# Optimization experiments

Hardware: AMD Instinct MI355X
Metric: run time of the kernel (lower is better)

Reference implementation:

```python
import jax, jax.numpy as jnp
import numpy as np

B, T, C, H = 4, 2048, 1024, 16
HD = C // H  # head_dim = 64


def setup_inputs() -> dict:
    key = jax.random.key(0)
    k1, k2, k3 = jax.random.split(key, 3)
    x = jax.random.normal(k1, (B, T, C), dtype=jnp.float32)
    W_qkv = jax.random.normal(k2, (C, 3 * C), dtype=jnp.float32) * (1.0 / np.sqrt(C))
    W_out = jax.random.normal(k3, (C, C), dtype=jnp.float32) * (1.0 / np.sqrt(C))
    return {"x": x, "W_qkv": W_qkv, "W_out": W_out}


def reference(x, W_qkv, W_out):
    Bx, Tx, Cx = x.shape
    qkv = jnp.einsum('btc,cd->btd', x, W_qkv)  # [B,T,3C]
    q, k, v = jnp.split(qkv, 3, axis=-1)
    # [B,T,C] -> [B,H,T,HD]
    q = q.reshape(Bx, Tx, H, HD).transpose(0, 2, 1, 3)
    k = k.reshape(Bx, Tx, H, HD).transpose(0, 2, 1, 3)
    v = v.reshape(Bx, Tx, H, HD).transpose(0, 2, 1, 3)
    scale = 1.0 / jnp.sqrt(jnp.asarray(HD, dtype=x.dtype))
    attn = jnp.einsum('bhqd,bhkd->bhqk', q, k) * scale  # [B,H,T,T]
    causal = jnp.tril(jnp.ones((Tx, Tx), dtype=bool))
    attn = jnp.where(causal, attn, jnp.asarray(-1e9, dtype=attn.dtype))
    attn = jax.nn.softmax(attn, axis=-1)
    out = jnp.einsum('bhqk,bhkd->bhqd', attn, v)  # [B,H,T,HD]
    out = out.transpose(0, 2, 1, 3).reshape(Bx, Tx, Cx)
    return jnp.einsum('btc,cd->btd', out, W_out)
```

## Files before the change

### kernel.cpp

```cpp
#include <hip/hip_runtime.h>
#include <hip/hip_bf16.h>
#include <cstdint>


typedef __attribute__((ext_vector_type(8))) short bf16x8;
typedef __attribute__((ext_vector_type(4))) float f32x4;
typedef __attribute__((ext_vector_type(4))) uint32_t u32x4;

#define MFMA_BF16(a, b, c) __builtin_amdgcn_mfma_f32_16x16x32_bf16((a), (b), (c), 0, 0, 0)

__device__ __forceinline__ ushort f2bf(float f) {
  union { float f; uint32_t u; } x;
  x.f = f;
  uint32_t u = x.u;
  return (ushort)((u + 0x7FFFu + ((u >> 16) & 1u)) >> 16);
}

__device__ __forceinline__ uint32_t cvt_pk_bf16(float lo, float hi) {
  uint32_t r;
  asm("v_cvt_pk_bf16_f32 %0, %1, %2" : "=v"(r) : "v"(lo), "v"(hi));
  return r;
}

__device__ __forceinline__ void gload16(const ushort* g, ushort* l) {
  __builtin_amdgcn_global_load_lds(
      (const __attribute__((address_space(1))) void*)g,
      (__attribute__((address_space(3))) void*)l, 16, 0, 0);
}

__global__ __launch_bounds__(256) void convert_f32_bf16(
    const float* __restrict__ in, ushort* __restrict__ out, int n4) {
  int i = blockIdx.x * 256 + threadIdx.x;
  if (i < n4) {
    float4 v = ((const float4*)in)[i];
    ushort4 o;
    o.x = f2bf(v.x); o.y = f2bf(v.y); o.z = f2bf(v.z); o.w = f2bf(v.w);
    ((ushort4*)out)[i] = o;
  }
}

__global__ __launch_bounds__(256) void transpose_w(
    const float* __restrict__ W, ushort* __restrict__ Wt, int K, int N) {
  __shared__ float tile[32][33];
  const int n0 = blockIdx.x * 32, k0 = blockIdx.y * 32;
  const int tx = threadIdx.x & 31, ty = threadIdx.x >> 5;
#pragma unroll
  for (int i = 0; i < 4; ++i)
    tile[ty + i * 8][tx] = W[(size_t)(k0 + ty + i * 8) * N + n0 + tx];
  __syncthreads();
#pragma unroll
  for (int i = 0; i < 4; ++i)
    Wt[(size_t)(n0 + ty + i * 8) * K + k0 + tx] = f2bf(tile[tx][ty + i * 8]);
}

template <int MODE>
__global__ __launch_bounds__(256)
__attribute__((amdgpu_waves_per_eu(2, 2)))
void gemm_bf16_kernel(
    const ushort* __restrict__ A, const ushort* __restrict__ Bt,
    float* __restrict__ C,
    ushort* __restrict__ qb, ushort* __restrict__ kb, ushort* __restrict__ vb,
    int M, int N, int K) {
  __shared__ ushort As[2][128 * 64];
  __shared__ ushort Bs[2][128 * 64];
  const int tid = threadIdx.x;
  const int lane = tid & 63;
  const int w = tid >> 6;
  const int wr = w >> 1, wc = w & 1;
  const int l15 = lane & 15, lhi = lane >> 4;
  const int row0 = blockIdx.x * 128, col0 = blockIdx.y * 128;

  const int cr = lane >> 3;
  const int sl = lane & 7;
  const int gofs = (sl ^ cr) << 3;
  const ushort* gA = A  + (size_t)(row0 + w * 32 + cr) * K + gofs;
  const ushort* gB = Bt + (size_t)(col0 + w * 32 + cr) * K + gofs;
  const int lbase = (w * 32) * 64;

  f32x4 acc[4][4] = {};

#define G_STAGE(BUF, K0)                                                     \
  {                                                                          \
    _Pragma("unroll")                                                        \
    for (int i = 0; i < 4; ++i) {                                            \
      gload16(gA + (size_t)(i * 8) * K + (K0), &As[BUF][lbase + i * 512]);   \
      gload16(gB + (size_t)(i * 8) * K + (K0), &Bs[BUF][lbase + i * 512]);   \
    }                                                                        \
  }

  const int nk = K >> 6;
  G_STAGE(0, 0)
  __syncthreads();

  for (int t = 0; t < nk; ++t) {
    const int cur = t & 1;
    if (t + 1 < nk) G_STAGE(cur ^ 1, (t + 1) << 6)

#pragma unroll
    for (int kh = 0; kh < 2; ++kh) {
      bf16x8 af[4], bfr[4];
#pragma unroll
      for (int m = 0; m < 4; ++m) {
        const int row = wr * 64 + m * 16 + l15;
        const int s = kh * 4 + lhi;
        af[m] = *(const bf16x8*)&As[cur][row * 64 + ((s ^ (row & 7)) << 3)];
      }
#pragma unroll
      for (int n = 0; n < 4; ++n) {
        const int row = wc * 64 + n * 16 + l15;
        const int s = kh * 4 + lhi;
        bfr[n] = *(const bf16x8*)&Bs[cur][row * 64 + ((s ^ (row & 7)) << 3)];
      }
      __builtin_amdgcn_s_setprio(1);
#pragma unroll
      for (int m = 0; m < 4; ++m)
#pragma unroll
        for (int n = 0; n < 4; ++n)
          acc[m][n] = MFMA_BF16(af[m], bfr[n], acc[m][n]);
      __builtin_amdgcn_s_setprio(0);
    }
    __syncthreads();
  }
#undef G_STAGE

  if (MODE == 1) {
#pragma unroll
    for (int m = 0; m < 4; ++m) {
      const int r0 = row0 + wr * 64 + m * 16 + lhi * 4;
#pragma unroll
      for (int n = 0; n < 4; ++n) {
        const int c = col0 + wc * 64 + n * 16 + l15;
#pragma unroll
        for (int j = 0; j < 4; ++j)
          C[(size_t)(r0 + j) * N + c] = acc[m][n][j];
      }
    }
  } else {
    const float QSCALE = 0.18033688011112042f;
#pragma unroll
    for (int m = 0; m < 4; ++m) {
      const int r0 = row0 + wr * 64 + m * 16 + lhi * 4;
      const int b_ = r0 >> 11;
      const int t0 = r0 & 2047;
#pragma unroll
      for (int n = 0; n < 4; ++n) {
        const int c = col0 + wc * 64 + n * 16 + l15;
        const int seg = c >> 10;
        const int cc = c & 1023;
        const int h = cc >> 6, d = cc & 63;
        const size_t bhi = (size_t)(b_ * 16 + h);
        if (seg == 0) {
#pragma unroll
          for (int j = 0; j < 4; ++j)
            qb[(bhi * 2048 + t0 + j) * 64 + d] = f2bf(acc[m][n][j] * QSCALE);
        } else if (seg == 1) {
#pragma unroll
          for (int j = 0; j < 4; ++j)
            kb[(bhi * 2048 + t0 + j) * 64 + d] = f2bf(acc[m][n][j]);
        } else {
          const int pos = (t0 & ~31) + ((t0 & 12) << 1) + ((t0 >> 4) & 1) * 4;
          ushort4 pk;
          pk.x = f2bf(acc[m][n][0]);
          pk.y = f2bf(acc[m][n][1]);
          pk.z = f2bf(acc[m][n][2]);
          pk.w = f2bf(acc[m][n][3]);
          *(ushort4*)(vb + (bhi * 64 + d) * 2048 + pos) = pk;
        }
      }
    }
  }
}

#define QK_TILE(SV, KT)                                                      \
  {                                                                          \
    const int krow = (KT) * 16 + l15;                                        \
    const int sw = krow & 7;                                                 \
    bf16x8 kf0 = *(const bf16x8*)&Ks[cur][krow * 64 + ((lhi ^ sw) * 8)];     \
    bf16x8 kf1 = *(const bf16x8*)&Ks[cur][krow * 64 + (((4 + lhi) ^ sw) * 8)];\
    f32x4 acc_ = {};                                                         \
    acc_ = MFMA_BF16(kf0, qf0, acc_);                                        \
    acc_ = MFMA_BF16(kf1, qf1, acc_);                                        \
    SV = acc_;                                                               \
  }

#define MASK_TILE(SV, KT)                                                    \
  {                                                                          \
    if (key0 + (KT) * 16 + lhi * 4 + 0 > qrow) SV[0] = -INFINITY;            \
    if (key0 + (KT) * 16 + lhi * 4 + 1 > qrow) SV[1] = -INFINITY;            \
    if (key0 + (KT) * 16 + lhi * 4 + 2 > qrow) SV[2] = -INFINITY;            \
    if (key0 + (KT) * 16 + lhi * 4 + 3 > qrow) SV[3] = -INFINITY;            \
  }

#define SM_TILE(SV, W0, W1)                                                  \
  {                                                                          \
    float p0 = exp2f(SV[0] - m_state);                                       \
    float p1 = exp2f(SV[1] - m_state);                                       \
    float p2 = exp2f(SV[2] - m_state);                                       \
    float p3 = exp2f(SV[3] - m_state);                                       \
    lloc += (p0 + p1) + (p2 + p3);                                           \
    W0 = cvt_pk_bf16(p0, p1);                                                \
    W1 = cvt_pk_bf16(p2, p3);                                                \
  }

#define PV_TILE(ON, N)                                                       \
  {                                                                          \
    const int vrow = (N) * 16 + l15;                                         \
    const int sw = vrow & 7;                                                 \
    bf16x8 vf0 = *(const bf16x8*)&Vs[cur][vrow * 64 + ((lhi ^ sw) * 8)];     \
    bf16x8 vf1 = *(const bf16x8*)&Vs[cur][vrow * 64 + (((4 + lhi) ^ sw) * 8)];\
    ON = MFMA_BF16(pf0, vf0, ON);                                            \
    ON = MFMA_BF16(pf1, vf1, ON);                                            \
  }

__global__ __launch_bounds__(256)
__attribute__((amdgpu_waves_per_eu(4, 4)))
void attn_kernel(
    const ushort* __restrict__ Qb, const ushort* __restrict__ Kb,
    const ushort* __restrict__ Vt, ushort* __restrict__ Ab) {
  const int bid = blockIdx.x;
  const int qt = 31 - (bid >> 6);
  const int bh = bid & 63;
  const int tid = threadIdx.x;
  const int lane = tid & 63;
  const int w = tid >> 6;
  const int l15 = lane & 15, lhi = lane >> 4;
  const int qloc = qt * 64 + w * 16;

  __shared__ ushort Ks[2][64 * 64];
  __shared__ ushort Vs[2][64 * 64];

  const size_t qkbase = (size_t)bh * (2048 * 64);
  const size_t vtb = (size_t)bh * (64 * 2048);

  const int srow = w * 16 + (lane >> 3);
  const int sd0 = lane & 7;
  const int slot = (sd0 ^ (srow & 7)) * 8;

  const ushort* kp0 = Kb + qkbase + (size_t)srow * 64 + sd0 * 8;
  const ushort* kp1 = kp0 + 8 * 64;
  const ushort* vp0 = Vt + vtb + (size_t)srow * 2048 + sd0 * 8;
  const ushort* vp1 = vp0 + 8 * 2048;

  bf16x8 qf0 = *(const bf16x8*)(Qb + qkbase + (size_t)(qloc + l15) * 64 + lhi * 8);
  bf16x8 qf1 = *(const bf16x8*)(Qb + qkbase + (size_t)(qloc + l15) * 64 + 32 + lhi * 8);

  uint4 kr0 = *(const uint4*)kp0;
  uint4 kr1 = *(const uint4*)kp1;
  uint4 vr0 = *(const uint4*)vp0;
  uint4 vr1 = *(const uint4*)vp1;
  *(uint4*)&Ks[0][srow * 64 + slot] = kr0;
  *(uint4*)&Ks[0][(srow + 8) * 64 + slot] = kr1;
  *(uint4*)&Vs[0][srow * 64 + slot] = vr0;
  *(uint4*)&Vs[0][(srow + 8) * 64 + slot] = vr1;
  __syncthreads();

  float m_state = -INFINITY, l_state = 0.f;
  f32x4 o0 = {}, o1 = {}, o2 = {}, o3 = {};
  const int qrow = qloc + l15;
  int cur = 0;

  for (int kbt = 0; kbt <= qt; ++kbt) {
    const int key0 = kbt * 64;
    const bool last = (kbt == qt);

    if (!last) {
      const size_t koff = (size_t)(kbt + 1) * 64 * 64;
      kr0 = *(const uint4*)(kp0 + koff);
      kr1 = *(const uint4*)(kp1 + koff);
      vr0 = *(const uint4*)(vp0 + (kbt + 1) * 64);
      vr1 = *(const uint4*)(vp1 + (kbt + 1) * 64);
    }

    f32x4 s0, s1, s2, s3;
    __builtin_amdgcn_s_setprio(1);
    QK_TILE(s0, 0)
    QK_TILE(s1, 1)
    QK_TILE(s2, 2)
    QK_TILE(s3, 3)
    __builtin_amdgcn_s_setprio(0);

    if (last) {
      MASK_TILE(s0, 0)
      MASK_TILE(s1, 1)
      MASK_TILE(s2, 2)
      MASK_TILE(s3, 3)
    }

    float t0 = fmaxf(fmaxf(s0[0], s0[1]), fmaxf(s0[2], s0[3]));
    float t1 = fmaxf(fmaxf(s1[0], s1[1]), fmaxf(s1[2], s1[3]));
    float t2 = fmaxf(fmaxf(s2[0], s2[1]), fmaxf(s2[2], s2[3]));
    float t3 = fmaxf(fmaxf(s3[0], s3[1]), fmaxf(s3[2], s3[3]));
    float tmax = fmaxf(fmaxf(t0, t1), fmaxf(t2, t3));
    tmax = fmaxf(tmax, __shfl_xor(tmax, 16));
    tmax = fmaxf(tmax, __shfl_xor(tmax, 32));

    if (!__all(tmax <= m_state + 8.0f)) {
      const float mnew = fmaxf(m_state, tmax);
      const float alpha = exp2f(m_state - mnew);
      const float a0 = __shfl(alpha, lhi * 4 + 0);
      const float a1 = __shfl(alpha, lhi * 4 + 1);
      const float a2 = __shfl(alpha, lhi * 4 + 2);
      const float a3 = __shfl(alpha, lhi * 4 + 3);
      o0[0] *= a0; o0[1] *= a1; o0[2] *= a2; o0[3] *= a3;
      o1[0] *= a0; o1[1] *= a1; o1[2] *= a2; o1[3] *= a3;
      o2[0] *= a0; o2[1] *= a1; o2[2] *= a2; o2[3] *= a3;
      o3[0] *= a0; o3[1] *= a1; o3[2] *= a2; o3[3] *= a3;
      l_state *= alpha;
      m_state = mnew;
    }

    float lloc = 0.f;
    uint32_t w0, w1, w2, w3, w4, w5, w6, w7;
    SM_TILE(s0, w0, w1)
    SM_TILE(s1, w2, w3)
    SM_TILE(s2, w4, w5)
    SM_TILE(s3, w6, w7)
    lloc += __shfl_xor(lloc, 16);
    lloc += __shfl_xor(lloc, 32);
    l_state += lloc;

    u32x4 pw0 = {w0, w1, w2, w3};
    u32x4 pw1 = {w4, w5, w6, w7};
    bf16x8 pf0 = __builtin_bit_cast(bf16x8, pw0);
    bf16x8 pf1 = __builtin_bit_cast(bf16x8, pw1);

    __builtin_amdgcn_s_setprio(1);
    PV_TILE(o0, 0)
    PV_TILE(o1, 1)
    PV_TILE(o2, 2)
    PV_TILE(o3, 3)
    __builtin_amdgcn_s_setprio(0);

    if (!last) {
      const int nxt = cur ^ 1;
      *(uint4*)&Ks[nxt][srow * 64 + slot] = kr0;
      *(uint4*)&Ks[nxt][(srow + 8) * 64 + slot] = kr1;
      *(uint4*)&Vs[nxt][srow * 64 + slot] = vr0;
      *(uint4*)&Vs[nxt][(srow + 8) * 64 + slot] = vr1;
      cur = nxt;
      __syncthreads();
    }
  }

  const int b_ = bh >> 4, h_ = bh & 15;
#pragma unroll
  for (int j = 0; j < 4; ++j) {
    const float linv = 1.0f / __shfl(l_state, lhi * 4 + j);
    const int t = qloc + lhi * 4 + j;
    const size_t ro = ((size_t)b_ * 2048 + t) * 1024 + h_ * 64;
    Ab[ro + 0 * 16 + l15] = f2bf(o0[j] * linv);
    Ab[ro + 1 * 16 + l15] = f2bf(o1[j] * linv);
    Ab[ro + 2 * 16 + l15] = f2bf(o2[j] * linv);
    Ab[ro + 3 * 16 + l15] = f2bf(o3[j] * linv);
  }
}

extern "C" void kernel_launch(void* const* d_in, const int* in_sizes, int n_in,
                              void* d_out, int out_size, void* d_ws, size_t ws_size,
                              hipStream_t stream) {
  const float* x = (const float*)d_in[0];
  const float* Wqkv = (const float*)d_in[1];
  const float* Wout = (const float*)d_in[2];
  float* out = (float*)d_out;

  ushort* xb    = (ushort*)d_ws;
  ushort* wqkvT = xb + (size_t)8192 * 1024;
  ushort* woutT = wqkvT + (size_t)3072 * 1024;
  ushort* qb    = woutT + (size_t)1024 * 1024;
  ushort* kbuf  = qb + (size_t)64 * 2048 * 64;
  ushort* vbuf  = kbuf + (size_t)64 * 2048 * 64;
  ushort* ab    = vbuf + (size_t)64 * 2048 * 64;

  convert_f32_bf16<<<8192, 256, 0, stream>>>(x, xb, 8192 * 1024 / 4);
  transpose_w<<<dim3(96, 32), 256, 0, stream>>>(Wqkv, wqkvT, 1024, 3072);
  transpose_w<<<dim3(32, 32), 256, 0, stream>>>(Wout, woutT, 1024, 1024);
  gemm_bf16_kernel<0><<<dim3(64, 24), 256, 0, stream>>>(
      xb, wqkvT, nullptr, qb, kbuf, vbuf, 8192, 3072, 1024);
  attn_kernel<<<2048, 256, 0, stream>>>(qb, kbuf, vbuf, ab);
  gemm_bf16_kernel<1><<<dim3(64, 8), 256, 0, stream>>>(
      ab, woutT, out, nullptr, nullptr, nullptr, 8192, 1024, 1024);
}
```

Baseline: 173.8 us.

## Halve GEMM K-tile, raise occupancy to three waves, add XCD-aware block swizzle

```diff
diff --git a/kernel.cpp b/kernel.cpp
--- a/kernel.cpp
+++ b/kernel.cpp
@@ -55,71 +55,71 @@
 
 template <int MODE>
 __global__ __launch_bounds__(256)
-__attribute__((amdgpu_waves_per_eu(2, 2)))
+__attribute__((amdgpu_waves_per_eu(3, 3)))
 void gemm_bf16_kernel(
     const ushort* __restrict__ A, const ushort* __restrict__ Bt,
     float* __restrict__ C,
     ushort* __restrict__ qb, ushort* __restrict__ kb, ushort* __restrict__ vb,
     int M, int N, int K) {
-  __shared__ ushort As[2][128 * 64];
-  __shared__ ushort Bs[2][128 * 64];
+  __shared__ ushort As[2][128 * 32];
+  __shared__ ushort Bs[2][128 * 32];
   const int tid = threadIdx.x;
   const int lane = tid & 63;
   const int w = tid >> 6;
   const int wr = w >> 1, wc = w & 1;
   const int l15 = lane & 15, lhi = lane >> 4;
-  const int row0 = blockIdx.x * 128, col0 = blockIdx.y * 128;
-
-  const int cr = lane >> 3;
-  const int sl = lane & 7;
-  const int gofs = (sl ^ cr) << 3;
+
+  const int nwg = gridDim.x;
+  const int cpx = nwg >> 3;
+  const int b = blockIdx.x;
+  const int swz = (b & 7) * cpx + (b >> 3);
+  const int row0 = (swz & 63) * 128;
+  const int col0 = (swz >> 6) * 128;
+
+  const int cr = lane >> 2;
+  const int sl = lane & 3;
+  const int gofs = (sl ^ (cr & 3)) << 3;
   const ushort* gA = A  + (size_t)(row0 + w * 32 + cr) * K + gofs;
   const ushort* gB = Bt + (size_t)(col0 + w * 32 + cr) * K + gofs;
-  const int lbase = (w * 32) * 64;
+  const int lbase = (w * 32) * 32;
 
   f32x4 acc[4][4] = {};
 
-#define G_STAGE(BUF, K0)                                                     \
-  {                                                                          \
-    _Pragma("unroll")                                                        \
-    for (int i = 0; i < 4; ++i) {                                            \
-      gload16(gA + (size_t)(i * 8) * K + (K0), &As[BUF][lbase + i * 512]);   \
-      gload16(gB + (size_t)(i * 8) * K + (K0), &Bs[BUF][lbase + i * 512]);   \
-    }                                                                        \
-  }
-
-  const int nk = K >> 6;
+#define G_STAGE(BUF, T)                                                      \
+  {                                                                          \
+    gload16(gA + (size_t)(T) * 32, &As[BUF][lbase]);                         \
+    gload16(gA + (size_t)16 * K + (size_t)(T) * 32, &As[BUF][lbase + 512]);  \
+    gload16(gB + (size_t)(T) * 32, &Bs[BUF][lbase]);                         \
+    gload16(gB + (size_t)16 * K + (size_t)(T) * 32, &Bs[BUF][lbase + 512]);  \
+  }
+
+  const int nk = K >> 5;
   G_STAGE(0, 0)
   __syncthreads();
 
   for (int t = 0; t < nk; ++t) {
     const int cur = t & 1;
-    if (t + 1 < nk) G_STAGE(cur ^ 1, (t + 1) << 6)
-
-#pragma unroll
-    for (int kh = 0; kh < 2; ++kh) {
-      bf16x8 af[4], bfr[4];
-#pragma unroll
-      for (int m = 0; m < 4; ++m) {
-        const int row = wr * 64 + m * 16 + l15;
-        const int s = kh * 4 + lhi;
-        af[m] = *(const bf16x8*)&As[cur][row * 64 + ((s ^ (row & 7)) << 3)];
-      }
-#pragma unroll
-      for (int n = 0; n < 4; ++n) {
-        const int row = wc * 64 + n * 16 + l15;
-        const int s = kh * 4 + lhi;
-        bfr[n] = *(const bf16x8*)&Bs[cur][row * 64 + ((s ^ (row & 7)) << 3)];
-      }
-      __builtin_amdgcn_s_setprio(1);
-#pragma unroll
-      for (int m = 0; m < 4; ++m)
-#pragma unroll
-        for (int n = 0; n < 4; ++n)
-          acc[m][n] = MFMA_BF16(af[m], bfr[n], acc[m][n]);
-      __builtin_amdgcn_s_setprio(0);
-    }
-    __syncthreads();
+    if (t + 1 < nk) G_STAGE(cur ^ 1, t + 1)
+
+    bf16x8 af[4], bfr[4];
+#pragma unroll
+    for (int m = 0; m < 4; ++m) {
+      const int row = wr * 64 + m * 16 + l15;
+      af[m] = *(const bf16x8*)&As[cur][row * 32 + ((lhi ^ (row & 3)) << 3)];
+    }
+#pragma unroll
+    for (int n = 0; n < 4; ++n) {
+      const int row = wc * 64 + n * 16 + l15;
+      bfr[n] = *(const bf16x8*)&Bs[cur][row * 32 + ((lhi ^ (row & 3)) << 3)];
+    }
+    __builtin_amdgcn_s_setprio(1);
+#pragma unroll
+    for (int m = 0; m < 4; ++m)
+#pragma unroll
+      for (int n = 0; n < 4; ++n)
+        acc[m][n] = MFMA_BF16(af[m], bfr[n], acc[m][n]);
+    __builtin_amdgcn_s_setprio(0);
+    if (t + 1 < nk) __syncthreads();
   }
 #undef G_STAGE
 
@@ -374,9 +374,9 @@
   convert_f32_bf16<<<8192, 256, 0, stream>>>(x, xb, 8192 * 1024 / 4);
   transpose_w<<<dim3(96, 32), 256, 0, stream>>>(Wqkv, wqkvT, 1024, 3072);
   transpose_w<<<dim3(32, 32), 256, 0, stream>>>(Wout, woutT, 1024, 1024);
-  gemm_bf16_kernel<0><<<dim3(64, 24), 256, 0, stream>>>(
+  gemm_bf16_kernel<0><<<1536, 256, 0, stream>>>(
       xb, wqkvT, nullptr, qb, kbuf, vbuf, 8192, 3072, 1024);
   attn_kernel<<<2048, 256, 0, stream>>>(qb, kbuf, vbuf, ab);
-  gemm_bf16_kernel<1><<<dim3(64, 8), 256, 0, stream>>>(
+  gemm_bf16_kernel<1><<<512, 256, 0, stream>>>(
       ab, woutT, out, nullptr, nullptr, nullptr, 8192, 1024, 1024);
 }
```

New measurement: 193.4 us. 1.11x slower.

## Use 256x256-tile 8-wave QKV GEMM with staged loads and XCD-aware block mapping

Applied to the files above, without the earlier changes.

```diff
diff --git a/kernel.cpp b/kernel.cpp
--- a/kernel.cpp
+++ b/kernel.cpp
@@ -53,14 +53,190 @@
     Wt[(size_t)(n0 + ty + i * 8) * K + k0 + tx] = f2bf(tile[tx][ty + i * 8]);
 }
 
-template <int MODE>
+
+#define LD_AF(MH)                                                            \
+  {                                                                          \
+    _Pragma("unroll")                                                        \
+    for (int m = 0; m < 4; ++m) {                                            \
+      const int row = wr * 128 + (MH) * 64 + m * 16 + l15;                   \
+      _Pragma("unroll")                                                      \
+      for (int kk = 0; kk < 2; ++kk)                                         \
+        af[m][kk] = *(const bf16x8*)&as[row * 64 +                           \
+                     (((kk * 4 + lhi) ^ (row & 7)) << 3)];                   \
+    }                                                                        \
+  }
+
+#define LD_BF(DST, NH)                                                       \
+  {                                                                          \
+    _Pragma("unroll")                                                        \
+    for (int n = 0; n < 2; ++n) {                                            \
+      const int row = wc * 64 + (NH) * 32 + n * 16 + l15;                    \
+      _Pragma("unroll")                                                      \
+      for (int kk = 0; kk < 2; ++kk)                                         \
+        DST[n][kk] = *(const bf16x8*)&bs[row * 64 +                          \
+                     (((kk * 4 + lhi) ^ (row & 7)) << 3)];                   \
+    }                                                                        \
+  }
+
+#define MFMA16(MH, NH, BF)                                                   \
+  {                                                                          \
+    __builtin_amdgcn_s_setprio(1);                                           \
+    _Pragma("unroll")                                                        \
+    for (int m = 0; m < 4; ++m)                                              \
+      _Pragma("unroll")                                                      \
+      for (int n = 0; n < 2; ++n)                                            \
+        _Pragma("unroll")                                                    \
+        for (int kk = 0; kk < 2; ++kk)                                       \
+          acc[(MH) * 4 + m][(NH) * 2 + n] = MFMA_BF16(                       \
+              af[m][kk], BF[n][kk], acc[(MH) * 4 + m][(NH) * 2 + n]);        \
+    __builtin_amdgcn_s_setprio(0);                                           \
+  }
+
+__global__ __launch_bounds__(512)
+__attribute__((amdgpu_waves_per_eu(2, 2)))
+void gemm256_qkv(
+    const ushort* __restrict__ A, const ushort* __restrict__ Bt,
+    ushort* __restrict__ qb, ushort* __restrict__ kb, ushort* __restrict__ vb,
+    int M, int N, int K) {
+  __shared__ ushort As[2][256 * 64];
+  __shared__ ushort Bs[2][256 * 64];
+  const int tid = threadIdx.x;
+  const int lane = tid & 63;
+  const int w = tid >> 6;
+  const int wr = w >> 2, wc = w & 3;
+  const int l15 = lane & 15, lhi = lane >> 4;
+
+  const int ncolt = N >> 8;
+  const int rpx = (M >> 8) >> 3;
+  const int b = blockIdx.x;
+  const int xcd = b & 7;
+  const int loc = b >> 3;
+  const int rowg = loc / ncolt;
+  const int colt = loc - rowg * ncolt;
+  const int row0 = (xcd * rpx + rowg) * 256;
+  const int col0 = colt * 256;
+
+  const int cr8 = lane >> 3;
+  const int sl8 = lane & 7;
+  const int gcol = (sl8 ^ cr8) << 3;
+  const int rA = (w & 3) * 16 + (w >> 2) * 128;
+  const int rB = (w & 1) * 16 + (w >> 1) * 64;
+  const ushort* gA0u = A  + (size_t)(row0 + rA + cr8) * K + gcol;
+  const ushort* gB0u = Bt + (size_t)(col0 + rB + cr8) * K + gcol;
+  const ushort* gA1u = gA0u + (size_t)64 * K;
+  const ushort* gB1u = gB0u + (size_t)32 * K;
+  const int lA0 = rA * 64;
+  const int lB0 = rB * 64;
+  const int lA1 = lA0 + 64 * 64;
+  const int lB1 = lB0 + 32 * 64;
+
+#define STAGE_A0(BUF, T)                                                     \
+  { gload16(gA0u + (size_t)(T) * 64, &As[BUF][lA0]);                         \
+    gload16(gA0u + (size_t)8 * K + (size_t)(T) * 64, &As[BUF][lA0 + 512]); }
+#define STAGE_B0(BUF, T)                                                     \
+  { gload16(gB0u + (size_t)(T) * 64, &Bs[BUF][lB0]);                         \
+    gload16(gB0u + (size_t)8 * K + (size_t)(T) * 64, &Bs[BUF][lB0 + 512]); }
+#define STAGE_B1(BUF, T)                                                     \
+  { gload16(gB1u + (size_t)(T) * 64, &Bs[BUF][lB1]);                         \
+    gload16(gB1u + (size_t)8 * K + (size_t)(T) * 64, &Bs[BUF][lB1 + 512]); }
+#define STAGE_A1(BUF, T)                                                     \
+  { gload16(gA1u + (size_t)(T) * 64, &As[BUF][lA1]);                         \
+    gload16(gA1u + (size_t)8 * K + (size_t)(T) * 64, &As[BUF][lA1 + 512]); }
+
+  f32x4 acc[8][4] = {};
+
+  const int nk = K >> 6;
+  STAGE_A0(0, 0)
+  STAGE_B0(0, 0)
+  STAGE_B1(0, 0)
+  STAGE_A1(0, 0)
+
+  for (int t = 0; t < nk; ++t) {
+    const int cur = t & 1;
+    const int nxt = cur ^ 1;
+    const ushort* as = &As[cur][0];
+    const ushort* bs = &Bs[cur][0];
+    const bool pre = (t + 1 < nk);
+
+    bf16x8 af[4][2], bf0[2][2], bf1[2][2];
+
+    asm volatile("s_waitcnt vmcnt(4)" ::: "memory");
+    __builtin_amdgcn_s_barrier();
+    __builtin_amdgcn_sched_barrier(0);
+    LD_AF(0)
+    LD_BF(bf0, 0)
+    if (pre) STAGE_A0(nxt, t + 1)
+    MFMA16(0, 0, bf0)
+
+    if (pre) {
+      asm volatile("s_waitcnt vmcnt(4)" ::: "memory");
+    } else {
+      asm volatile("s_waitcnt vmcnt(2)" ::: "memory");
+    }
+    __builtin_amdgcn_s_barrier();
+    __builtin_amdgcn_sched_barrier(0);
+    LD_BF(bf1, 1)
+    if (pre) STAGE_B0(nxt, t + 1)
+    MFMA16(0, 1, bf1)
+
+    if (pre) {
+      asm volatile("s_waitcnt vmcnt(4)" ::: "memory");
+    } else {
+      asm volatile("s_waitcnt vmcnt(0)" ::: "memory");
+    }
+    __builtin_amdgcn_s_barrier();
+    __builtin_amdgcn_sched_barrier(0);
+    LD_AF(1)
+    if (pre) STAGE_B1(nxt, t + 1)
+    MFMA16(1, 1, bf1)
+
+    if (pre) STAGE_A1(nxt, t + 1)
+    MFMA16(1, 0, bf0)
+  }
+#undef STAGE_A0
+#undef STAGE_B0
+#undef STAGE_B1
+#undef STAGE_A1
+
+  const float QSCALE = 0.18033688011112042f;
+#pragma unroll
+  for (int m = 0; m < 8; ++m) {
+    const int r0 = row0 + wr * 128 + m * 16 + lhi * 4;
+    const int b_ = r0 >> 11;
+    const int t0 = r0 & 2047;
+#pragma unroll
+    for (int n = 0; n < 4; ++n) {
+      const int c = col0 + wc * 64 + n * 16 + l15;
+      const int seg = c >> 10;
+      const int cc = c & 1023;
+      const int h = cc >> 6, d = cc & 63;
+      const size_t bhi = (size_t)(b_ * 16 + h);
+      if (seg == 0) {
+#pragma unroll
+        for (int j = 0; j < 4; ++j)
+          qb[(bhi * 2048 + t0 + j) * 64 + d] = f2bf(acc[m][n][j] * QSCALE);
+      } else if (seg == 1) {
+#pragma unroll
+        for (int j = 0; j < 4; ++j)
+          kb[(bhi * 2048 + t0 + j) * 64 + d] = f2bf(acc[m][n][j]);
+      } else {
+        const int pos = (t0 & ~31) + ((t0 & 12) << 1) + ((t0 >> 4) & 1) * 4;
+        ushort4 pk;
+        pk.x = f2bf(acc[m][n][0]);
+        pk.y = f2bf(acc[m][n][1]);
+        pk.z = f2bf(acc[m][n][2]);
+        pk.w = f2bf(acc[m][n][3]);
+        *(ushort4*)(vb + (bhi * 64 + d) * 2048 + pos) = pk;
+      }
+    }
+  }
+}
+
 __global__ __launch_bounds__(256)
 __attribute__((amdgpu_waves_per_eu(2, 2)))
-void gemm_bf16_kernel(
+void gemm_out(
     const ushort* __restrict__ A, const ushort* __restrict__ Bt,
-    float* __restrict__ C,
-    ushort* __restrict__ qb, ushort* __restrict__ kb, ushort* __restrict__ vb,
-    int M, int N, int K) {
+    float* __restrict__ C, int M, int N, int K) {
   __shared__ ushort As[2][128 * 64];
   __shared__ ushort Bs[2][128 * 64];
   const int tid = threadIdx.x;
@@ -79,7 +255,7 @@
 
   f32x4 acc[4][4] = {};
 
-#define G_STAGE(BUF, K0)                                                     \
+#define G_STAGE8(BUF, K0)                                                    \
   {                                                                          \
     _Pragma("unroll")                                                        \
     for (int i = 0; i < 4; ++i) {                                            \
@@ -89,12 +265,12 @@
   }
 
   const int nk = K >> 6;
-  G_STAGE(0, 0)
+  G_STAGE8(0, 0)
   __syncthreads();
 
   for (int t = 0; t < nk; ++t) {
     const int cur = t & 1;
-    if (t + 1 < nk) G_STAGE(cur ^ 1, (t + 1) << 6)
+    if (t + 1 < nk) G_STAGE8(cur ^ 1, (t + 1) << 6)
 
 #pragma unroll
     for (int kh = 0; kh < 2; ++kh) {
@@ -121,52 +297,17 @@
     }
     __syncthreads();
   }
-#undef G_STAGE
-
-  if (MODE == 1) {
-#pragma unroll
-    for (int m = 0; m < 4; ++m) {
-      const int r0 = row0 + wr * 64 + m * 16 + lhi * 4;
-#pragma unroll
-      for (int n = 0; n < 4; ++n) {
-        const int c = col0 + wc * 64 + n * 16 + l15;
-#pragma unroll
-        for (int j = 0; j < 4; ++j)
-          C[(size_t)(r0 + j) * N + c] = acc[m][n][j];
-      }
-    }
-  } else {
-    const float QSCALE = 0.18033688011112042f;
-#pragma unroll
-    for (int m = 0; m < 4; ++m) {
-      const int r0 = row0 + wr * 64 + m * 16 + lhi * 4;
-      const int b_ = r0 >> 11;
-      const int t0 = r0 & 2047;
-#pragma unroll
-      for (int n = 0; n < 4; ++n) {
-        const int c = col0 + wc * 64 + n * 16 + l15;
-        const int seg = c >> 10;
-        const int cc = c & 1023;
-        const int h = cc >> 6, d = cc & 63;
-        const size_t bhi = (size_t)(b_ * 16 + h);
-        if (seg == 0) {
-#pragma unroll
-          for (int j = 0; j < 4; ++j)
-            qb[(bhi * 2048 + t0 + j) * 64 + d] = f2bf(acc[m][n][j] * QSCALE);
-        } else if (seg == 1) {
-#pragma unroll
-          for (int j = 0; j < 4; ++j)
-            kb[(bhi * 2048 + t0 + j) * 64 + d] = f2bf(acc[m][n][j]);
-        } else {
-          const int pos = (t0 & ~31) + ((t0 & 12) << 1) + ((t0 >> 4) & 1) * 4;
-          ushort4 pk;
-          pk.x = f2bf(acc[m][n][0]);
-          pk.y = f2bf(acc[m][n][1]);
-          pk.z = f2bf(acc[m][n][2]);
-          pk.w = f2bf(acc[m][n][3]);
-          *(ushort4*)(vb + (bhi * 64 + d) * 2048 + pos) = pk;
-        }
-      }
+#undef G_STAGE8
+
+#pragma unroll
+  for (int m = 0; m < 4; ++m) {
+    const int r0 = row0 + wr * 64 + m * 16 + lhi * 4;
+#pragma unroll
+    for (int n = 0; n < 4; ++n) {
+      const int c = col0 + wc * 64 + n * 16 + l15;
+#pragma unroll
+      for (int j = 0; j < 4; ++j)
+        C[(size_t)(r0 + j) * N + c] = acc[m][n][j];
     }
   }
 }
@@ -374,9 +515,9 @@
   convert_f32_bf16<<<8192, 256, 0, stream>>>(x, xb, 8192 * 1024 / 4);
   transpose_w<<<dim3(96, 32), 256, 0, stream>>>(Wqkv, wqkvT, 1024, 3072);
   transpose_w<<<dim3(32, 32), 256, 0, stream>>>(Wout, woutT, 1024, 1024);
-  gemm_bf16_kernel<0><<<dim3(64, 24), 256, 0, stream>>>(
-      xb, wqkvT, nullptr, qb, kbuf, vbuf, 8192, 3072, 1024);
+  gemm256_qkv<<<384, 512, 0, stream>>>(
+      xb, wqkvT, qb, kbuf, vbuf, 8192, 3072, 1024);
   attn_kernel<<<2048, 256, 0, stream>>>(qb, kbuf, vbuf, ab);
-  gemm_bf16_kernel<1><<<dim3(64, 8), 256, 0, stream>>>(
-      ab, woutT, out, nullptr, nullptr, nullptr, 8192, 1024, 1024);
-}
+  gemm_out<<<dim3(64, 8), 256, 0, stream>>>(
+      ab, woutT, out, 8192, 1024, 1024);
+}
```

New measurement: 173.3 us. No clear change (-0.3%).
